# Performance work log

Hardware: AMD Instinct MI355X
Metric: run time of the kernel (lower is better)

The kernel has to match this reference:

```python
import jax, jax.numpy as jnp
import numpy as np

N = 100000      # nodes
E = 1600000     # edges
IN_F = 128
CL1 = 64
CL2 = 64
OUT_F = 2
G = 128         # graphs in batch


def setup_inputs() -> dict:
    key = jax.random.key(0)
    ks = jax.random.split(key, 9)
    x = jax.random.normal(ks[0], (N, IN_F), dtype=jnp.float32)
    edge_index = jax.random.randint(ks[1], (2, E), 0, N, dtype=jnp.int64)
    batch = jnp.sort(jax.random.randint(ks[2], (N,), 0, G, dtype=jnp.int64))
    # Glorot-ish init for GCN weights, PyG Linear-style for the head
    W1 = jax.random.normal(ks[3], (IN_F, CL1), dtype=jnp.float32) / np.sqrt(IN_F)
    b1 = jnp.zeros((CL1,), dtype=jnp.float32)
    W2 = jax.random.normal(ks[4], (CL1, CL2), dtype=jnp.float32) / np.sqrt(CL1)
    b2 = jnp.zeros((CL2,), dtype=jnp.float32)
    Wlin = jax.random.normal(ks[5], (CL2 * 3, OUT_F), dtype=jnp.float32) / np.sqrt(CL2 * 3)
    blin = jnp.zeros((OUT_F,), dtype=jnp.float32)
    return dict(x=x, W1=W1, b1=b1, W2=W2, b2=b2, Wlin=Wlin, blin=blin,
                edge_index=edge_index, batch=batch, num_graphs=G)


def gcn_conv(x, src, dst, W, b):
    """PyG GCNConv: add self-loops, symmetric normalization, x@W, scatter-add, +bias."""
    n = x.shape[0]
    xw = x @ W  # [N, out_c] -- transform BEFORE propagate (PyG order)
    loop = jnp.arange(n, dtype=src.dtype)
    s = jnp.concatenate([src, loop])  # sources incl. self loops
    d = jnp.concatenate([dst, loop])  # destinations incl. self loops
    deg = jax.ops.segment_sum(jnp.ones(s.shape, x.dtype), d, num_segments=n)
    dinv = jnp.where(deg > 0, jax.lax.rsqrt(deg), 0.0)
    norm = dinv[s] * dinv[d]                      # [E+N]
    msg = xw[s] * norm[:, None]                   # gather + scale
    return jax.ops.segment_sum(msg, d, num_segments=n) + b


def reference(x, W1, b1, W2, b2, Wlin, blin, edge_index, batch, num_graphs):
    src, dst = edge_index[0], edge_index[1]
    h = jax.nn.relu(gcn_conv(x, src, dst, W1, b1))
    h = jax.nn.relu(gcn_conv(h, src, dst, W2, b2))
    # global add / mean / max pooling over graphs
    x0 = jax.ops.segment_sum(h, batch, num_segments=num_graphs)
    cnt = jax.ops.segment_sum(jnp.ones((h.shape[0],), h.dtype), batch, num_segments=num_graphs)
    x1 = x0 / jnp.maximum(cnt, 1.0)[:, None]
    x2 = jax.ops.segment_max(h, batch, num_segments=num_graphs)
    x2 = jnp.where(jnp.isfinite(x2), x2, 0.0)  # empty segments -> 0
    xcat = jnp.concatenate([x0, x1, x2], axis=-1)  # [G, 3*CL2]
    out = xcat @ Wlin + blin                       # [G, OUT_F]
    return (xcat, out)
```

## Files before the change

### kernel.cpp

```cpp
#include <hip/hip_runtime.h>

#define IN_F 128
#define C1 64
#define NG 128
#define CAT 192
#define DCAP 10240

typedef unsigned short u16;
typedef unsigned char u8;
typedef unsigned int u32;
typedef __attribute__((ext_vector_type(8))) short bf16x8;
typedef __attribute__((ext_vector_type(4))) float f32x4;

__device__ inline u16 f2bf(float f) {
  u32 u = __float_as_uint(f);
  u = (u + 0x7FFFu + ((u >> 16) & 1u)) >> 16;
  return (u16)u;
}
__device__ inline float bf2f(u16 h) { return __uint_as_float(((u32)h) << 16); }
__device__ inline float bflo(u32 p) { return __uint_as_float(p << 16); }
__device__ inline float bfhi(u32 p) { return __uint_as_float(p & 0xFFFF0000u); }


__global__ void zero_k(int* __restrict__ g) { g[threadIdx.x] = 0; }


__global__ __launch_bounds__(256) void stage_k(const int* __restrict__ src,
                                               const int* __restrict__ dst, int e,
                                               int* __restrict__ gcur,
                                               u32* __restrict__ stage, int ndig) {
  __shared__ int h4[4][256];
  __shared__ int sc[256];
  __shared__ int lcur[256];
  __shared__ int loff[256];
  __shared__ u32 ebuf[4096];
  __shared__ u8  dbuf[4096];
  int t = threadIdx.x;
  int wv = t >> 6;
  h4[0][t] = 0; h4[1][t] = 0; h4[2][t] = 0; h4[3][t] = 0;
  __syncthreads();
  int base = blockIdx.x * 4096;
  int tot = min(4096, e - base);
  int mys[16], myd[16];
  #pragma unroll
  for (int i = 0; i < 16; i++) {
    int j = base + t + i * 256;
    if (j < e) {
      mys[i] = src[j];
      myd[i] = dst[j];
      atomicAdd(&h4[wv][myd[i] >> 9], 1);
    } else {
      myd[i] = -1;
    }
  }
  __syncthreads();
  int cnt = h4[0][t] + h4[1][t] + h4[2][t] + h4[3][t];
  sc[t] = cnt;
  __syncthreads();
  #pragma unroll
  for (int off = 1; off < 256; off <<= 1) {
    int x = sc[t] + ((t >= off) ? sc[t - off] : 0);
    __syncthreads();
    sc[t] = x;
    __syncthreads();
  }
  int excl = sc[t] - cnt;
  int gbase = 0;
  if (t < ndig && cnt > 0) gbase = atomicAdd(&gcur[t], cnt);
  lcur[t] = excl;
  loff[t] = t * DCAP + gbase - excl;
  __syncthreads();
  #pragma unroll
  for (int i = 0; i < 16; i++) {
    if (myd[i] >= 0) {
      int d = myd[i] >> 9;
      int r = atomicAdd(&lcur[d], 1);
      ebuf[r] = (u32)mys[i] | ((u32)(myd[i] & 511) << 17);
      dbuf[r] = (u8)d;
    }
  }
  __syncthreads();
  for (int j = t; j < tot; j += 256) {
    int d = dbuf[j];
    stage[loff[d] + j] = ebuf[j];
  }
}

__global__ __launch_bounds__(256) void csr_k(const u32* __restrict__ stage,
                                             const int* __restrict__ gcur,
                                             int* __restrict__ rowptr,
                                             int* __restrict__ counts,
                                             float* __restrict__ dinv,
                                             int* __restrict__ csr, int n) {
  __shared__ int hc[512];
  __shared__ int hb[512];
  __shared__ int cu[512];
  __shared__ int sc[256];
  __shared__ u32 lbuf[DCAP];
  int dg = blockIdx.x;
  int t = threadIdx.x;
  int n0 = dg * 512;
  int nloc = min(n - n0, 512);
  int e0 = dg * DCAP;
  int cntE = gcur[dg];
  hc[t] = 0; hc[t + 256] = 0;
  __syncthreads();
  for (int j = t; j < cntE; j += 256) atomicAdd(&hc[stage[e0 + j] >> 17], 1);
  __syncthreads();
  int a0 = hc[2 * t], a1 = hc[2 * t + 1];
  int s = a0 + a1;
  sc[t] = s;
  __syncthreads();
  #pragma unroll
  for (int off = 1; off < 256; off <<= 1) {
    int x = sc[t] + ((t >= off) ? sc[t - off] : 0);
    __syncthreads();
    sc[t] = x;
    __syncthreads();
  }
  int excl = sc[t] - s;
  hb[2 * t] = excl;
  hb[2 * t + 1] = excl + a0;
  cu[2 * t] = 0; cu[2 * t + 1] = 0;
  __syncthreads();
  for (int i = t; i < nloc; i += 256) {
    int node = n0 + i;
    rowptr[node] = e0 + hb[i];
    counts[node] = hc[i];
    dinv[node] = rsqrtf((float)hc[i] + 1.0f);
  }
  __syncthreads();
  for (int j = t; j < cntE; j += 256) {
    u32 p = stage[e0 + j];
    int li = p >> 17;
    int r = atomicAdd(&cu[li], 1);
    lbuf[hb[li] + r] = p & 0x1FFFFu;
  }
  __syncthreads();
  for (int j = t; j < cntE; j += 256) csr[e0 + j] = (int)lbuf[j];
}


template <int K, bool IN_BF16>
__global__ __launch_bounds__(256) void gemm_mfma_k(const void* __restrict__ Xv,
                                                   const float* __restrict__ W,
                                                   const float* __restrict__ dinv,
                                                   u16* __restrict__ Y, int n) {
  constexpr int KK = K / 32;
  constexpr int XSN = 2048 * KK;
  constexpr int TOT = 4096 * KK;
  constexpr int SMEMN = (TOT > 9216) ? TOT : 9216;
  __shared__ u16 smem[SMEMN];
  u16* Xs = smem;
  u16* Ws = smem + XSN;
  int t = threadIdx.x;
  int row0 = blockIdx.x * 64;

  for (int idx = t; idx < K * 16; idx += 256) {
    int k = idx >> 4, c4 = (idx & 15) * 4;
    float4 wv = *(const float4*)(W + (size_t)k * 64 + c4);
    int kk = k >> 5, k8 = (k & 31) >> 3, kr = k & 7;
    float wa[4] = {wv.x, wv.y, wv.z, wv.w};
    #pragma unroll
    for (int j = 0; j < 4; j++) {
      int c = c4 + j;
      u32 byte = (u32)(((kk * 64 + c) * 32 + k8 * 8 + kr) * 2);
      byte ^= (u32)((c & 7) << 4);
      *(u16*)((char*)Ws + byte) = f2bf(wa[j]);
    }
  }

  for (int idx = t; idx < 8 * K; idx += 256) {
    int r = idx / (K / 8);
    int c8 = idx % (K / 8);
    int gr = row0 + r;
    u16 vals[8];
    if (gr < n) {
      if (IN_BF16) {
        *(uint4*)vals = *(const uint4*)((const u16*)Xv + (size_t)gr * K + c8 * 8);
      } else {
        const float4 x0 = *(const float4*)((const float*)Xv + (size_t)gr * K + c8 * 8);
        const float4 x1 = *(const float4*)((const float*)Xv + (size_t)gr * K + c8 * 8 + 4);
        vals[0] = f2bf(x0.x); vals[1] = f2bf(x0.y); vals[2] = f2bf(x0.z); vals[3] = f2bf(x0.w);
        vals[4] = f2bf(x1.x); vals[5] = f2bf(x1.y); vals[6] = f2bf(x1.z); vals[7] = f2bf(x1.w);
      }
    } else {
      #pragma unroll
      for (int j = 0; j < 8; j++) vals[j] = 0;
    }
    int wrow = r >> 4, row = r & 15, kk = c8 >> 2, k8 = c8 & 3;
    u32 byte = (u32)((((wrow * KK + kk) * 16 + row) * 32 + k8 * 8) * 2);
    byte ^= (u32)((row & 7) << 4);
    *(uint4*)((char*)Xs + byte) = *(uint4*)vals;
  }
  __syncthreads();

  int w = t >> 6, l = t & 63;
  int lrow = l & 15, lk = l >> 4;
  bf16x8 bfrag[KK][4];
  #pragma unroll
  for (int kk = 0; kk < KK; kk++) {
    #pragma unroll
    for (int cb = 0; cb < 4; cb++) {
      int col = cb * 16 + lrow;
      u32 byte = (u32)(((kk * 64 + col) * 32 + lk * 8) * 2);
      byte ^= (u32)((col & 7) << 4);
      bfrag[kk][cb] = *(bf16x8*)((char*)Ws + byte);
    }
  }
  f32x4 acc[4] = {};
  #pragma unroll
  for (int kk = 0; kk < KK; kk++) {
    u32 abyte = (u32)((((w * KK + kk) * 16 + lrow) * 32 + lk * 8) * 2);
    abyte ^= (u32)((lrow & 7) << 4);
    bf16x8 a = *(bf16x8*)((char*)Xs + abyte);
    #pragma unroll
    for (int cb = 0; cb < 4; cb++) {
      acc[cb] = __builtin_amdgcn_mfma_f32_16x16x32_bf16(a, bfrag[kk][cb], acc[cb], 0, 0, 0);
    }
  }
  __syncthreads();

  float dv[4];
  #pragma unroll
  for (int reg = 0; reg < 4; reg++) {
    int gr = row0 + w * 16 + lk * 4 + reg;
    dv[reg] = (gr < n) ? dinv[gr] : 0.f;
  }
  #pragma unroll
  for (int cb = 0; cb < 4; cb++) {
    #pragma unroll
    for (int reg = 0; reg < 4; reg++) {
      int r = w * 16 + lk * 4 + reg;
      int c = cb * 16 + lrow;
      smem[r * 72 + c] = f2bf(acc[cb][reg] * dv[reg]);
    }
  }
  __syncthreads();
  #pragma unroll
  for (int p = 0; p < 2; p++) {
    int idx = t + p * 256;
    int rr = idx >> 3, ch = idx & 7;
    int gr = row0 + rr;
    if (gr < n) {
      uint4 v = *(uint4*)&smem[rr * 72 + ch * 8];
      *(uint4*)(Y + (size_t)gr * 64 + ch * 8) = v;
    }
  }
}


__device__ __forceinline__ void gather_node(const u16* __restrict__ xw,
                                            const int* __restrict__ rowptr,
                                            const int* __restrict__ counts,
                                            const int* __restrict__ csr,
                                            const float* __restrict__ dinv,
                                            const float* __restrict__ bias,
                                            int nid, int lane, float acc[8]) {
  {
    uint4 a = *(const uint4*)(xw + (size_t)nid * 64 + lane * 8);
    acc[0] = bflo(a.x); acc[1] = bfhi(a.x);
    acc[2] = bflo(a.y); acc[3] = bfhi(a.y);
    acc[4] = bflo(a.z); acc[5] = bfhi(a.z);
    acc[6] = bflo(a.w); acc[7] = bfhi(a.w);
  }
  int st = rowptr[nid];
  int cn = counts[nid];
  int mi = (lane < cn) ? csr[st + lane] : 0;
  for (int c = 0; c < cn; c += 8) {
    int rem = cn - c;
    uint4 vv[8];
    #pragma unroll
    for (int i = 0; i < 8; i++) {
      int s = __shfl(mi, i, 8);
      if (i < rem) {
        vv[i] = *(const uint4*)(xw + (size_t)s * 64 + lane * 8);
      } else {
        vv[i] = make_uint4(0, 0, 0, 0);
      }
    }
    int nmi = (c + 8 + lane < cn) ? csr[st + c + 8 + lane] : 0;
    #pragma unroll
    for (int i = 0; i < 8; i++) {
      acc[0] += bflo(vv[i].x); acc[1] += bfhi(vv[i].x);
      acc[2] += bflo(vv[i].y); acc[3] += bfhi(vv[i].y);
      acc[4] += bflo(vv[i].z); acc[5] += bfhi(vv[i].z);
      acc[6] += bflo(vv[i].w); acc[7] += bfhi(vv[i].w);
    }
    mi = nmi;
  }
  float di = dinv[nid];
  const float4 b0 = *(const float4*)(bias + lane * 8);
  const float4 b1 = *(const float4*)(bias + lane * 8 + 4);
  acc[0] = fmaxf(acc[0] * di + b0.x, 0.f);
  acc[1] = fmaxf(acc[1] * di + b0.y, 0.f);
  acc[2] = fmaxf(acc[2] * di + b0.z, 0.f);
  acc[3] = fmaxf(acc[3] * di + b0.w, 0.f);
  acc[4] = fmaxf(acc[4] * di + b1.x, 0.f);
  acc[5] = fmaxf(acc[5] * di + b1.y, 0.f);
  acc[6] = fmaxf(acc[6] * di + b1.z, 0.f);
  acc[7] = fmaxf(acc[7] * di + b1.w, 0.f);
}

__global__ __launch_bounds__(256) void gather_k(const u16* __restrict__ xw,
                                                u16* __restrict__ hout,
                                                const int* __restrict__ rowptr,
                                                const int* __restrict__ counts,
                                                const int* __restrict__ csr,
                                                const float* __restrict__ dinv,
                                                const float* __restrict__ bias, int n) {
  int idx = blockIdx.x * 256 + threadIdx.x;
  int nid = idx >> 3;
  int lane = idx & 7;
  if (nid >= n) return;
  float acc[8];
  gather_node(xw, rowptr, counts, csr, dinv, bias, nid, lane, acc);
  uint4 o;
  o.x = ((u32)f2bf(acc[0])) | ((u32)f2bf(acc[1]) << 16);
  o.y = ((u32)f2bf(acc[2])) | ((u32)f2bf(acc[3]) << 16);
  o.z = ((u32)f2bf(acc[4])) | ((u32)f2bf(acc[5]) << 16);
  o.w = ((u32)f2bf(acc[6])) | ((u32)f2bf(acc[7]) << 16);
  *(uint4*)(hout + (size_t)nid * 64 + lane * 8) = o;
}


__global__ __launch_bounds__(1024) void pool_k(const u16* __restrict__ h,
                                               const int* __restrict__ batch, int n,
                                               const float* __restrict__ Wlin,
                                               const float* __restrict__ blin,
                                               float* __restrict__ xcat,
                                               float* __restrict__ outh) {
  int g = blockIdx.x;
  __shared__ int se[2];
  if (threadIdx.x < 2) {
    int target = g + (int)threadIdx.x;
    int lo = 0, hi = n;
    while (lo < hi) {
      int mid = (lo + hi) >> 1;
      if (batch[mid] < target) lo = mid + 1; else hi = mid;
    }
    se[threadIdx.x] = lo;
  }
  __syncthreads();
  int s = se[0], e = se[1];
  int lane = threadIdx.x & 63;
  int wv = threadIdx.x >> 6;
  float sum = 0.f, mx = 0.f;
  for (int nn = s + wv; nn < e; nn += 16) {
    float v = bf2f(h[(size_t)nn * 64 + lane]);
    sum += v;
    mx = fmaxf(mx, v);
  }
  __shared__ float lsum[16][64];
  __shared__ float lmax[16][64];
  lsum[wv][lane] = sum;
  lmax[wv][lane] = mx;
  __syncthreads();
  if (wv == 0) {
    #pragma unroll
    for (int i = 1; i < 16; i++) {
      sum += lsum[i][lane];
      mx = fmaxf(mx, lmax[i][lane]);
    }
    int cnt = e - s;
    float x0 = sum;
    float x1 = sum / fmaxf((float)cnt, 1.0f);
    float x2 = mx;
    xcat[g * CAT + lane]       = x0;
    xcat[g * CAT + 64 + lane]  = x1;
    xcat[g * CAT + 128 + lane] = x2;
    #pragma unroll
    for (int o = 0; o < 2; o++) {
      float p = x0 * Wlin[lane * 2 + o] +
                x1 * Wlin[(64 + lane) * 2 + o] +
                x2 * Wlin[(128 + lane) * 2 + o];
      #pragma unroll
      for (int off = 32; off > 0; off >>= 1) p += __shfl_down(p, off, 64);
      if (lane == 0) outh[g * 2 + o] = p + blin[o];
    }
  }
}


extern "C" void kernel_launch(void* const* d_in, const int* in_sizes, int n_in,
                              void* d_out, int out_size, void* d_ws, size_t ws_size,
                              hipStream_t stream) {
  const float* x    = (const float*)d_in[0];
  const float* W1   = (const float*)d_in[1];
  const float* b1   = (const float*)d_in[2];
  const float* W2   = (const float*)d_in[3];
  const float* b2   = (const float*)d_in[4];
  const float* Wlin = (const float*)d_in[5];
  const float* blin = (const float*)d_in[6];
  const int*   ei   = (const int*)d_in[7];
  const int*   batch= (const int*)d_in[8];

  const int N = in_sizes[0] / IN_F;
  const int E = in_sizes[7] / 2;
  const int* src = ei;
  const int* dst = ei + E;
  const int ndig = (N + 511) >> 9;
  const int nbE  = (E + 4095) / 4096;

  char* w = (char*)d_ws;
  auto alloc = [&](size_t bytes) {
    void* p = (void*)w;
    w += (bytes + 255) & ~(size_t)255;
    return p;
  };
  int*   rowptr = (int*)alloc((size_t)N * 4);
  int*   counts = (int*)alloc((size_t)N * 4);
  float* dinv   = (float*)alloc((size_t)N * 4);
  int*   csr    = (int*)alloc((size_t)ndig * DCAP * 4);
  int*   gcur   = (int*)alloc(256 * 4);
  u16*   bufA   = (u16*)alloc((size_t)N * 64 * 2);
  u16*   bufB   = (u16*)alloc((size_t)N * 64 * 2);
  u32*   stage  = (u32*)alloc((size_t)ndig * DCAP * 4);

  float* xcat = (float*)d_out;
  float* outh = (float*)d_out + NG * CAT;

  zero_k  <<<1, 256, 0, stream>>>(gcur);
  stage_k <<<nbE, 256, 0, stream>>>(src, dst, E, gcur, stage, ndig);
  csr_k   <<<ndig, 256, 0, stream>>>(stage, gcur, rowptr, counts, dinv, csr, N);

  gemm_mfma_k<IN_F, false> <<<(N + 63) / 64, 256, 0, stream>>>(x, W1, dinv, bufA, N);
  gather_k <<<(N * 8 + 255) / 256, 256, 0, stream>>>(bufA, bufB, rowptr, counts, csr, dinv, b1, N);

  gemm_mfma_k<C1, true> <<<(N + 63) / 64, 256, 0, stream>>>(bufB, W2, dinv, bufA, N);
  gather_k <<<(N * 8 + 255) / 256, 256, 0, stream>>>(bufA, bufB, rowptr, counts, csr, dinv, b2, N);

  pool_k <<<NG, 1024, 0, stream>>>(bufB, batch, N, Wlin, blin, xcat, outh);
}
```

Baseline: 151.2 us.

## Split pooling across four blocks per graph, per-wave bucket cursors, prescaled CSR offsets

Pooling now launches four blocks per graph, each covering a quarter of the graph's nodes. Partial sums and maxes are combined with global atomics into zeroed buffers, and a new finalize kernel computes the mean, the xcat output and the linear head. The edge staging kernel gives each wave its own bucket cursors, so shared-memory atomics on the same counter no longer collide across waves. CSR entries are stored pre-shifted as byte offsets, which removes the multiply from the gather's address calculation. The costs are an extra kernel launch, a larger zeroing pass, and float atomics whose summation order is not deterministic.

```diff
diff --git a/kernel.cpp b/kernel.cpp
--- a/kernel.cpp
+++ b/kernel.cpp
@@ -22,7 +22,10 @@
 __device__ inline float bfhi(u32 p) { return __uint_as_float(p & 0xFFFF0000u); }
 
 
-__global__ void zero_k(int* __restrict__ g) { g[threadIdx.x] = 0; }
+__global__ void zero_k(int* __restrict__ g, int n) {
+  int i = blockIdx.x * 256 + threadIdx.x;
+  if (i < n) g[i] = 0;
+}
 
 
 __global__ __launch_bounds__(256) void stage_k(const int* __restrict__ src,
@@ -31,7 +34,7 @@
                                                u32* __restrict__ stage, int ndig) {
   __shared__ int h4[4][256];
   __shared__ int sc[256];
-  __shared__ int lcur[256];
+  __shared__ int lcur4[4][256];
   __shared__ int loff[256];
   __shared__ u32 ebuf[4096];
   __shared__ u8  dbuf[4096];
@@ -67,14 +70,17 @@
   int excl = sc[t] - cnt;
   int gbase = 0;
   if (t < ndig && cnt > 0) gbase = atomicAdd(&gcur[t], cnt);
-  lcur[t] = excl;
+  lcur4[0][t] = excl;
+  lcur4[1][t] = excl + h4[0][t];
+  lcur4[2][t] = excl + h4[0][t] + h4[1][t];
+  lcur4[3][t] = excl + h4[0][t] + h4[1][t] + h4[2][t];
   loff[t] = t * DCAP + gbase - excl;
   __syncthreads();
   #pragma unroll
   for (int i = 0; i < 16; i++) {
     if (myd[i] >= 0) {
       int d = myd[i] >> 9;
-      int r = atomicAdd(&lcur[d], 1);
+      int r = atomicAdd(&lcur4[wv][d], 1);
       ebuf[r] = (u32)mys[i] | ((u32)(myd[i] & 511) << 17);
       dbuf[r] = (u8)d;
     }
@@ -134,7 +140,7 @@
     u32 p = stage[e0 + j];
     int li = p >> 17;
     int r = atomicAdd(&cu[li], 1);
-    lbuf[hb[li] + r] = p & 0x1FFFFu;
+    lbuf[hb[li] + r] = (p & 0x1FFFFu) << 7;
   }
   __syncthreads();
   for (int j = t; j < cntE; j += 256) csr[e0 + j] = (int)lbuf[j];
@@ -267,6 +273,7 @@
   int st = rowptr[nid];
   int cn = counts[nid];
   int mi = (lane < cn) ? csr[st + lane] : 0;
+  const char* xwb = (const char*)xw + lane * 16;
   for (int c = 0; c < cn; c += 8) {
     int rem = cn - c;
     uint4 vv[8];
@@ -274,7 +281,7 @@
     for (int i = 0; i < 8; i++) {
       int s = __shfl(mi, i, 8);
       if (i < rem) {
-        vv[i] = *(const uint4*)(xw + (size_t)s * 64 + lane * 8);
+        vv[i] = *(const uint4*)(xwb + (u32)s);
       } else {
         vv[i] = make_uint4(0, 0, 0, 0);
       }
@@ -326,11 +333,10 @@
 
 __global__ __launch_bounds__(1024) void pool_k(const u16* __restrict__ h,
                                                const int* __restrict__ batch, int n,
-                                               const float* __restrict__ Wlin,
-                                               const float* __restrict__ blin,
-                                               float* __restrict__ xcat,
-                                               float* __restrict__ outh) {
-  int g = blockIdx.x;
+                                               float* __restrict__ gsum,
+                                               u32* __restrict__ gmax) {
+  int g = blockIdx.x >> 2;
+  int q = blockIdx.x & 3;
   __shared__ int se[2];
   if (threadIdx.x < 2) {
     int target = g + (int)threadIdx.x;
@@ -342,11 +348,14 @@
     se[threadIdx.x] = lo;
   }
   __syncthreads();
-  int s = se[0], e = se[1];
+  int s0 = se[0], e0 = se[1];
+  int len = e0 - s0;
+  int qs = s0 + (int)(((long long)len * q) >> 2);
+  int qe = s0 + (int)(((long long)len * (q + 1)) >> 2);
   int lane = threadIdx.x & 63;
   int wv = threadIdx.x >> 6;
   float sum = 0.f, mx = 0.f;
-  for (int nn = s + wv; nn < e; nn += 16) {
+  for (int nn = qs + wv; nn < qe; nn += 16) {
     float v = bf2f(h[(size_t)nn * 64 + lane]);
     sum += v;
     mx = fmaxf(mx, v);
@@ -362,22 +371,47 @@
       sum += lsum[i][lane];
       mx = fmaxf(mx, lmax[i][lane]);
     }
-    int cnt = e - s;
-    float x0 = sum;
-    float x1 = sum / fmaxf((float)cnt, 1.0f);
-    float x2 = mx;
-    xcat[g * CAT + lane]       = x0;
-    xcat[g * CAT + 64 + lane]  = x1;
-    xcat[g * CAT + 128 + lane] = x2;
-    #pragma unroll
-    for (int o = 0; o < 2; o++) {
-      float p = x0 * Wlin[lane * 2 + o] +
-                x1 * Wlin[(64 + lane) * 2 + o] +
-                x2 * Wlin[(128 + lane) * 2 + o];
-      #pragma unroll
-      for (int off = 32; off > 0; off >>= 1) p += __shfl_down(p, off, 64);
-      if (lane == 0) outh[g * 2 + o] = p + blin[o];
-    }
+    if (sum != 0.f) atomicAdd(&gsum[g * 64 + lane], sum);
+    if (mx > 0.f) atomicMax(&gmax[g * 64 + lane], __float_as_uint(mx));
+  }
+}
+
+
+__global__ __launch_bounds__(64) void fin_k(const float* __restrict__ gsum,
+                                            const u32* __restrict__ gmax,
+                                            const int* __restrict__ batch, int n,
+                                            const float* __restrict__ Wlin,
+                                            const float* __restrict__ blin,
+                                            float* __restrict__ xcat,
+                                            float* __restrict__ outh) {
+  int g = blockIdx.x;
+  int lane = threadIdx.x;
+  __shared__ int se[2];
+  if (lane < 2) {
+    int target = g + lane;
+    int lo = 0, hi = n;
+    while (lo < hi) {
+      int mid = (lo + hi) >> 1;
+      if (batch[mid] < target) lo = mid + 1; else hi = mid;
+    }
+    se[lane] = lo;
+  }
+  __syncthreads();
+  int cnt = se[1] - se[0];
+  float x0 = gsum[g * 64 + lane];
+  float x1 = x0 / fmaxf((float)cnt, 1.0f);
+  float x2 = __uint_as_float(gmax[g * 64 + lane]);
+  xcat[g * CAT + lane]       = x0;
+  xcat[g * CAT + 64 + lane]  = x1;
+  xcat[g * CAT + 128 + lane] = x2;
+  #pragma unroll
+  for (int o = 0; o < 2; o++) {
+    float p = x0 * Wlin[lane * 2 + o] +
+              x1 * Wlin[(64 + lane) * 2 + o] +
+              x2 * Wlin[(128 + lane) * 2 + o];
+    #pragma unroll
+    for (int off = 32; off > 0; off >>= 1) p += __shfl_down(p, off, 64);
+    if (lane == 0) outh[g * 2 + o] = p + blin[o];
   }
 }
 
@@ -412,15 +446,20 @@
   int*   counts = (int*)alloc((size_t)N * 4);
   float* dinv   = (float*)alloc((size_t)N * 4);
   int*   csr    = (int*)alloc((size_t)ndig * DCAP * 4);
-  int*   gcur   = (int*)alloc(256 * 4);
+  int*   zbuf   = (int*)alloc((size_t)(256 + 2 * NG * 64) * 4);
   u16*   bufA   = (u16*)alloc((size_t)N * 64 * 2);
   u16*   bufB   = (u16*)alloc((size_t)N * 64 * 2);
   u32*   stage  = (u32*)alloc((size_t)ndig * DCAP * 4);
 
+  int*   gcur = zbuf;
+  float* gsum = (float*)(zbuf + 256);
+  u32*   gmax = (u32*)(zbuf + 256 + NG * 64);
+
   float* xcat = (float*)d_out;
   float* outh = (float*)d_out + NG * CAT;
 
-  zero_k  <<<1, 256, 0, stream>>>(gcur);
+  const int nz = 256 + 2 * NG * 64;
+  zero_k  <<<(nz + 255) / 256, 256, 0, stream>>>(zbuf, nz);
   stage_k <<<nbE, 256, 0, stream>>>(src, dst, E, gcur, stage, ndig);
   csr_k   <<<ndig, 256, 0, stream>>>(stage, gcur, rowptr, counts, dinv, csr, N);
 
@@ -430,5 +469,6 @@
   gemm_mfma_k<C1, true> <<<(N + 63) / 64, 256, 0, stream>>>(bufB, W2, dinv, bufA, N);
   gather_k <<<(N * 8 + 255) / 256, 256, 0, stream>>>(bufA, bufB, rowptr, counts, csr, dinv, b2, N);
 
-  pool_k <<<NG, 1024, 0, stream>>>(bufB, batch, N, Wlin, blin, xcat, outh);
-}
+  pool_k <<<NG * 4, 1024, 0, stream>>>(bufB, batch, N, gsum, gmax);
+  fin_k  <<<NG, 64, 0, stream>>>(gsum, gmax, batch, N, Wlin, blin, xcat, outh);
+}
```

After: 145.5 us. 1.04x faster.
